# Kernel tuning notes

Measured on AMD Instinct MI355X. Metric: run time of the kernel, lower is better.

## Reference

```python
import jax, jax.numpy as jnp
import numpy as np

D_MODEL = 1024
N_SA = 8          # self-attention heads
N_RA = 8          # relational-attention heads
TOTAL = N_SA + N_RA
HEAD_DIM = D_MODEL // TOTAL   # 64
KEY_DIM = HEAD_DIM            # default key_dim = d_model // total_n_heads
N_REL = 8                     # n_relations (= n_heads_ra default)
REL_PROJ = KEY_DIM            # rel_proj_dim default
B, S = 4, 1024


def _rope(x, cos, sin):
    # x: [b, s, h, d]; cos/sin: [s, d//2]; interleaved-pair rotation as in apply_rotary_emb
    xr = x.reshape(x.shape[:-1] + (-1, 2))
    x_r, x_i = xr[..., 0], xr[..., 1]
    c = cos[None, :, None, :]
    s = sin[None, :, None, :]
    o_r = x_r * c - x_i * s
    o_i = x_r * s + x_i * c
    return jnp.stack([o_r, o_i], axis=-1).reshape(x.shape)


def setup_inputs() -> dict:
    key = jax.random.key(0)
    ks = jax.random.split(key, 16)
    def p(k, shape, scale=0.02):
        return jax.random.normal(k, shape, dtype=jnp.float32) * scale
    x = jax.random.normal(ks[0], (B, S, D_MODEL), dtype=jnp.float32)
    symbols = jax.random.normal(ks[1], (B, S, D_MODEL), dtype=jnp.float32)
    # standard RoPE frequency tables, shape [S, KEY_DIM//2]
    inv_freq = 1.0 / (10000.0 ** (np.arange(0, KEY_DIM, 2, dtype=np.float32) / KEY_DIM))
    ang = np.outer(np.arange(S, dtype=np.float32), inv_freq)
    freqs_cos = jnp.asarray(np.cos(ang), dtype=jnp.float32)
    freqs_sin = jnp.asarray(np.sin(ang), dtype=jnp.float32)
    return dict(
        x=x, symbols=symbols, freqs_cos=freqs_cos, freqs_sin=freqs_sin,
        # self-attention stream params
        wq_sa=p(ks[2], (D_MODEL, N_SA * KEY_DIM)),
        wk_sa=p(ks[3], (D_MODEL, N_SA * KEY_DIM)),
        wv_sa=p(ks[4], (D_MODEL, N_SA * HEAD_DIM)),
        wo_sa=p(ks[5], (N_SA * HEAD_DIM, N_SA * HEAD_DIM)),
        # relational-attention stream params
        wq_attn=p(ks[6], (D_MODEL, N_RA * KEY_DIM)),
        wk_attn=p(ks[7], (D_MODEL, N_RA * KEY_DIM)),
        wq_rel=p(ks[8], (D_MODEL, N_REL * REL_PROJ)),
        wk_rel=p(ks[9], (D_MODEL, N_REL * REL_PROJ)),
        wr=p(ks[10], (N_RA, HEAD_DIM, N_REL)),      # per-head relation->head_dim map
        wv_sym=p(ks[11], (D_MODEL, N_RA * HEAD_DIM)),  # symbol projection
        wo_ra=p(ks[12], (N_RA * HEAD_DIM, N_RA * HEAD_DIM)),
    )


def reference(x, symbols, freqs_cos, freqs_sin, wq_sa, wk_sa, wv_sa, wo_sa,
              wq_attn, wk_attn, wq_rel, wk_rel, wr, wv_sym, wo_ra):
    b, s, _ = x.shape
    attn_scale = 1.0 / jnp.sqrt(jnp.asarray(HEAD_DIM, dtype=x.dtype))
    rel_scale = 1.0 / jnp.sqrt(jnp.asarray(REL_PROJ, dtype=x.dtype))
    causal = jnp.tril(jnp.ones((s, s), dtype=bool))
    neg = jnp.where(causal, jnp.asarray(0.0, x.dtype), jnp.asarray(-jnp.inf, x.dtype))

    # ---- standard self-attention stream ----
    q = _rope((x @ wq_sa).reshape(b, s, N_SA, KEY_DIM), freqs_cos, freqs_sin)
    k = _rope((x @ wk_sa).reshape(b, s, N_SA, KEY_DIM), freqs_cos, freqs_sin)
    v = (x @ wv_sa).reshape(b, s, N_SA, HEAD_DIM)
    scores = jnp.einsum('bihd,bjhd->bhij', q, k) * attn_scale + neg
    attn = jax.nn.softmax(scores, axis=-1)
    sa_out = jnp.einsum('bhij,bjhd->bihd', attn, v).reshape(b, s, -1) @ wo_sa

    # ---- relational attention stream ----
    qa = _rope((x @ wq_attn).reshape(b, s, N_RA, KEY_DIM), freqs_cos, freqs_sin)
    ka = _rope((x @ wk_attn).reshape(b, s, N_RA, KEY_DIM), freqs_cos, freqs_sin)
    ra_scores = jnp.einsum('bihd,bjhd->bhij', qa, ka) * attn_scale + neg
    ra_attn = jax.nn.softmax(ra_scores, axis=-1)
    # relations r(i,j) in R^{n_rel}: inner products of relation projections, tanh-activated
    qr = (x @ wq_rel).reshape(b, s, N_REL, REL_PROJ)
    kr = (x @ wk_rel).reshape(b, s, N_REL, REL_PROJ)
    rel = jnp.tanh(jnp.einsum('bird,bjrd->bijr', qr, kr) * rel_scale)  # [b,s,s,n_rel]
    sv = (symbols @ wv_sym).reshape(b, s, N_RA, HEAD_DIM)
    sym_msg = jnp.einsum('bhij,bjhd->bihd', ra_attn, sv)
    rel_msg = jnp.einsum('bhij,bijr->bihr', ra_attn, rel)
    rel_proj = jnp.einsum('bihr,hdr->bihd', rel_msg, wr)
    ra_out = (sym_msg + rel_proj).reshape(b, s, -1) @ wo_ra

    # dual attention: concat the two streams along feature dim -> [b, s, d_model]
    return jnp.concatenate([sa_out, ra_out], axis=-1)
```

## Files before the change

### kernel.cpp

```cpp
#include <hip/hip_runtime.h>

typedef unsigned short u16;
typedef unsigned int u32;
typedef __attribute__((ext_vector_type(4))) short s16x4;
typedef __attribute__((ext_vector_type(8))) short s16x8;
typedef __attribute__((ext_vector_type(4))) float f32x4;

#define C_QSA 0
#define C_KSA 512
#define C_VSA 1024
#define C_QA  1536
#define C_KA  2048
#define C_QR  2560
#define C_KR  3072
#define C_SV  3584
#define LDP   4096

__device__ __forceinline__ u16 f2bf(float f) {
    union { float f; unsigned u; } v; v.f = f;
    return (u16)((v.u + 0x7FFFu + ((v.u >> 16) & 1u)) >> 16);
}
__device__ __forceinline__ float bf2f(u16 h) {
    union { unsigned u; float f; } v; v.u = ((unsigned)h) << 16; return v.f;
}
__device__ __forceinline__ float fexp(float y) {
    return __builtin_exp2f(y * 1.4426950408889634f);
}
__device__ __forceinline__ float ftanh(float x) {
    float e = __builtin_exp2f(x * 2.885390081777927f);
    return 1.f - 2.f / (e + 1.f);
}
__device__ __forceinline__ f32x4 mfma16(s16x8 a, s16x8 b, f32x4 c) {
    return __builtin_amdgcn_mfma_f32_16x16x32_bf16(a, b, c, 0, 0, 0);
}
__device__ __forceinline__ void gload16(const u16* g, u16* l) {
    __builtin_amdgcn_global_load_lds(
        (const __attribute__((address_space(1))) void*)g,
        (__attribute__((address_space(3))) void*)l, 16, 0, 0);
}


__global__ void cvt_f32_bf16(const float* __restrict__ in, u16* __restrict__ out, int n) {
    int i = (blockIdx.x * 256 + threadIdx.x) * 8;
    if (i >= n) return;
    float4 a = *(const float4*)(in + i);
    float4 b = *(const float4*)(in + i + 4);
    s16x8 o;
    o[0] = (short)f2bf(a.x); o[1] = (short)f2bf(a.y);
    o[2] = (short)f2bf(a.z); o[3] = (short)f2bf(a.w);
    o[4] = (short)f2bf(b.x); o[5] = (short)f2bf(b.y);
    o[6] = (short)f2bf(b.z); o[7] = (short)f2bf(b.w);
    *(s16x8*)(out + i) = o;
}

struct WP { const float* p[10]; };

__global__ void transpose_w(WP wp, u16* __restrict__ WcatT,
                            u16* __restrict__ woSaT, u16* __restrict__ woRaT) {
    const int z = blockIdx.z;
    const float* W;
    u16* Wt;
    int K;
    if (z < 8) { W = wp.p[z]; Wt = WcatT + (size_t)z * 524288; K = 1024; }
    else       { W = wp.p[z]; Wt = (z == 8) ? woSaT : woRaT;   K = 512;  }
    const int N = 512;
    const int kt = blockIdx.x * 32, nt = blockIdx.y * 32;
    if (kt >= K) return;
    __shared__ float t[32][33];
    const int c = threadIdx.x & 31, r0 = threadIdx.x >> 5;
#pragma unroll
    for (int it = 0; it < 4; ++it) {
        int r = it * 8 + r0;
        t[r][c] = W[(size_t)(kt + r) * N + nt + c];
    }
    __syncthreads();
#pragma unroll
    for (int it = 0; it < 4; ++it) {
        int r = it * 8 + r0;
        Wt[(size_t)(nt + r) * K + kt + c] = f2bf(t[c][r]);
    }
}

__global__ void transpose_v2(const u16* __restrict__ P, u16* __restrict__ Vt, int colOff) {
    const int st = blockIdx.x * 32, ht = blockIdx.y * 32, b = blockIdx.z;
    __shared__ u16 t[32][34];
    const int c = threadIdx.x & 31, r0 = threadIdx.x >> 5;
#pragma unroll
    for (int it = 0; it < 4; ++it) {
        int r = it * 8 + r0;
        t[r][c] = P[(size_t)(b * 1024 + st + r) * LDP + colOff + ht + c];
    }
    __syncthreads();
    const int cp = ((c & 15) >> 2) * 8 + (c >> 4) * 4 + (c & 3);
#pragma unroll
    for (int it = 0; it < 4; ++it) {
        int r = it * 8 + r0;
        Vt[(size_t)b * 524288 + (size_t)(ht + r) * 1024 + st + cp] = t[c][r];
    }
}


__global__ void rope_kernel(u16* __restrict__ P, const float* __restrict__ fcos,
                            const float* __restrict__ fsin) {
    int idx = blockIdx.x * 256 + threadIdx.x;
    int row = idx >> 10;
    int rem = idx & 1023;
    int region = rem >> 8;
    int pr = rem & 255;
    int head = pr >> 5, p = pr & 31;
    int off = (region + (region >> 1)) * 512;
    int col = off + head * 64 + 2 * p;
    int s = row & 1023;
    float c = fcos[s * 32 + p], sn = fsin[s * 32 + p];
    u32* ptr = (u32*)(P + (size_t)row * LDP + col);
    u32 v = *ptr;
    float xr = bf2f((u16)(v & 0xffff)), xi = bf2f((u16)(v >> 16));
    u16 o0 = f2bf(xr * c - xi * sn);
    u16 o1 = f2bf(xr * sn + xi * c);
    *ptr = (u32)o0 | ((u32)o1 << 16);
}


template<bool OUT_BF16>
__global__ __launch_bounds__(256) void gemm_bf16(
    const u16* __restrict__ A, const u16* __restrict__ A2, int lda, int nswitch,
    const u16* __restrict__ Bt, int ldb,
    void* __restrict__ Cp, int ldc, int ccolOff, int K)
{
    __shared__ u16 As[128][32];
    __shared__ u16 Bs[128][32];
    const int tid = threadIdx.x;
    const int m0 = blockIdx.x * 128, n0 = blockIdx.y * 128;
    const u16* Ause = (A2 != nullptr && n0 >= nswitch) ? A2 : A;
    const int w = tid >> 6, lane = tid & 63;
    const int w32 = w * 32;
    const int wm = (w >> 1) * 64, wn = (w & 1) * 64;
    const int lr = lane & 15, lg = lane >> 4;
    const int lrow = lane >> 2;
    const int lseg = (lane & 3) * 8;
    f32x4 acc[4][4] = {};

    for (int k0 = 0; k0 < K; k0 += 32) {
        const u16* ga = &Ause[(size_t)(m0 + w32 + lrow) * lda + k0 + lseg];
        const u16* gb = &Bt [(size_t)(n0 + w32 + lrow) * ldb + k0 + lseg];
        gload16(ga,            &As[w32][0]);
        gload16(ga + 16 * lda, &As[w32 + 16][0]);
        gload16(gb,            &Bs[w32][0]);
        gload16(gb + 16 * ldb, &Bs[w32 + 16][0]);
        __syncthreads();
        s16x8 af[4], bfr[4];
#pragma unroll
        for (int t = 0; t < 4; ++t) {
            af[t]  = *(const s16x8*)&As[wm + t * 16 + lr][lg * 8];
            bfr[t] = *(const s16x8*)&Bs[wn + t * 16 + lr][lg * 8];
        }
#pragma unroll
        for (int i = 0; i < 4; ++i)
#pragma unroll
            for (int j = 0; j < 4; ++j)
                acc[i][j] = mfma16(af[i], bfr[j], acc[i][j]);
        __syncthreads();
    }
#pragma unroll
    for (int i = 0; i < 4; ++i)
#pragma unroll
        for (int j = 0; j < 4; ++j)
#pragma unroll
            for (int r = 0; r < 4; ++r) {
                int row = m0 + wm + i * 16 + lg * 4 + r;
                int col = n0 + wn + j * 16 + lr;
                float val = acc[i][j][r];
                if (OUT_BF16)
                    ((u16*)Cp)[(size_t)row * ldc + ccolOff + col] = f2bf(val);
                else
                    ((float*)Cp)[(size_t)row * ldc + ccolOff + col] = val;
            }
}


__global__ __launch_bounds__(64) void attn_sa(u16* __restrict__ P, const u16* __restrict__ Vt) {
    const int bid = blockIdx.x;
    const int h = bid & 7;
    const int b = (bid >> 3) & 3;
    const int pr = bid >> 5;
    const int xt1 = pr, xt2 = 63 - pr;
    const int lane = threadIdx.x, lr = lane & 15, lg = lane >> 4;
    const size_t rowBase = (size_t)b * 1024;
    const int i0_1 = xt1 * 16, i0_2 = xt2 * 16;
    const int ir1 = i0_1 + lr, ir2 = i0_2 + lr;

    const u16* Kbase = P + rowBase * LDP + (C_KSA + h * 64);
    const u16* Vb = Vt + ((size_t)(b * 8 + h)) * 65536;

    s16x8 q1[2], q2[2];
    {
        const u16* q = P + (rowBase + ir1) * LDP + (C_QSA + h * 64) + lg * 8;
        q1[0] = *(const s16x8*)q; q1[1] = *(const s16x8*)(q + 32);
        q = P + (rowBase + ir2) * LDP + (C_QSA + h * 64) + lg * 8;
        q2[0] = *(const s16x8*)q; q2[1] = *(const s16x8*)(q + 32);
    }
    f32x4 o1[4] = {}, o2[4] = {};
    float l1 = 0.f, l2 = 0.f;
    const int njt  = (xt2 >> 1) + 1;
    const int njt1 = (xt1 >> 1) + 1;

    for (int jt = 0; jt < njt; ++jt) {
        const int j0 = jt * 32;
        const bool act1 = (jt < njt1);
        s16x8 kf[2][2], vfr[4];
#pragma unroll
        for (int sub = 0; sub < 2; ++sub) {
            const u16* kp = Kbase + (size_t)(j0 + sub * 16 + lr) * LDP + lg * 8;
            kf[sub][0] = *(const s16x8*)kp;
            kf[sub][1] = *(const s16x8*)(kp + 32);
        }
#pragma unroll
        for (int ds = 0; ds < 4; ++ds)
            vfr[ds] = *(const s16x8*)(Vb + (size_t)(ds * 16 + lr) * 1024 + j0 + 8 * lg);

        f32x4 sc2[2] = {{0.f,0.f,0.f,0.f},{0.f,0.f,0.f,0.f}};
        f32x4 sc1[2] = {{0.f,0.f,0.f,0.f},{0.f,0.f,0.f,0.f}};
#pragma unroll
        for (int sub = 0; sub < 2; ++sub) {
            sc2[sub] = mfma16(kf[sub][0], q2[0], sc2[sub]);
            sc2[sub] = mfma16(kf[sub][1], q2[1], sc2[sub]);
        }
        if (act1) {
#pragma unroll
            for (int sub = 0; sub < 2; ++sub) {
                sc1[sub] = mfma16(kf[sub][0], q1[0], sc1[sub]);
                sc1[sub] = mfma16(kf[sub][1], q1[1], sc1[sub]);
            }
        }
        s16x8 pa;
#pragma unroll
        for (int sub = 0; sub < 2; ++sub)
#pragma unroll
            for (int r = 0; r < 4; ++r) {
                int j = j0 + sub * 16 + 4 * lg + r;
                float p = (j <= ir2) ? fexp(sc2[sub][r] * 0.125f) : 0.f;
                l2 += p;
                pa[sub * 4 + r] = (short)f2bf(p);
            }
#pragma unroll
        for (int ds = 0; ds < 4; ++ds) o2[ds] = mfma16(pa, vfr[ds], o2[ds]);
        if (act1) {
#pragma unroll
            for (int sub = 0; sub < 2; ++sub)
#pragma unroll
                for (int r = 0; r < 4; ++r) {
                    int j = j0 + sub * 16 + 4 * lg + r;
                    float p = (j <= ir1) ? fexp(sc1[sub][r] * 0.125f) : 0.f;
                    l1 += p;
                    pa[sub * 4 + r] = (short)f2bf(p);
                }
#pragma unroll
            for (int ds = 0; ds < 4; ++ds) o1[ds] = mfma16(pa, vfr[ds], o1[ds]);
        }
    }
    l1 += __shfl_xor(l1, 16); l1 += __shfl_xor(l1, 32);
    l2 += __shfl_xor(l2, 16); l2 += __shfl_xor(l2, 32);
    float li1[4], li2[4];
#pragma unroll
    for (int r = 0; r < 4; ++r) {
        li1[r] = 1.f / __shfl(l1, 4 * lg + r);
        li2[r] = 1.f / __shfl(l2, 4 * lg + r);
    }
#pragma unroll
    for (int ds = 0; ds < 4; ++ds)
#pragma unroll
        for (int r = 0; r < 4; ++r) {
            P[(rowBase + i0_1 + 4 * lg + r) * LDP + (C_QSA + h * 64) + ds * 16 + lr] =
                f2bf(o1[ds][r] * li1[r]);
            P[(rowBase + i0_2 + 4 * lg + r) * LDP + (C_QSA + h * 64) + ds * 16 + lr] =
                f2bf(o2[ds][r] * li2[r]);
        }
}


__global__ __launch_bounds__(512) void attn_ra(u16* __restrict__ P, const u16* __restrict__ SVt,
                                               float* __restrict__ opart,
                                               float* __restrict__ mlr) {
    const int bid = blockIdx.x;
    const int slot = bid & 7;
    const int b = slot & 3, s = slot >> 2;
    const int xt = 63 - (bid >> 3);
    const int w = threadIdx.x >> 6, lane = threadIdx.x & 63;
    const int lr = lane & 15, lg = lane >> 4;
    const int h = w;
    const size_t rowBase = (size_t)b * 1024;
    const int i0 = xt * 16;
    const int ir = i0 + lr;

    __shared__ float relT[2][2][32][16][8];

    const u16* Kbase  = P + rowBase * LDP + (C_KA + h * 64);
    const u16* KRbase = P + rowBase * LDP + (C_KR + h * 64);
    const u16* Vb = SVt + ((size_t)(b * 8 + h)) * 65536;

    s16x8 qf[2], qrf[2];
    {
        const u16* q = P + (rowBase + ir) * LDP + (C_QA + h * 64) + lg * 8;
        qf[0] = *(const s16x8*)q; qf[1] = *(const s16x8*)(q + 32);
        const u16* qr = P + (rowBase + ir) * LDP + (C_QR + h * 64) + lg * 8;
        qrf[0] = *(const s16x8*)qr; qrf[1] = *(const s16x8*)(qr + 32);
    }
    f32x4 o[4] = {};
    float rmr[8] = {};
    float l = 0.f;
    const int njt = (xt >> 1) + 1;
    const int cnt = (njt - s + 1) >> 1;
    const int npair = (cnt + 1) >> 1;
    const int slotw = (w + lr) & 7;

    for (int u = 0; u < npair; ++u) {
        const int j0a = (s + 4 * u) * 32;
        const bool actB = (2 * u + 1) < cnt;
        const int j0b = actB ? j0a + 64 : j0a;
        s16x8 kfA[2][2], krA[2][2], kfB[2][2], krB[2][2], vfA[4], vfB[4];
#pragma unroll
        for (int sub = 0; sub < 2; ++sub) {
            const u16* kp = Kbase + (size_t)(j0a + sub * 16 + lr) * LDP + lg * 8;
            kfA[sub][0] = *(const s16x8*)kp;  kfA[sub][1] = *(const s16x8*)(kp + 32);
            const u16* krp = KRbase + (size_t)(j0a + sub * 16 + lr) * LDP + lg * 8;
            krA[sub][0] = *(const s16x8*)krp; krA[sub][1] = *(const s16x8*)(krp + 32);
            kp = Kbase + (size_t)(j0b + sub * 16 + lr) * LDP + lg * 8;
            kfB[sub][0] = *(const s16x8*)kp;  kfB[sub][1] = *(const s16x8*)(kp + 32);
            krp = KRbase + (size_t)(j0b + sub * 16 + lr) * LDP + lg * 8;
            krB[sub][0] = *(const s16x8*)krp; krB[sub][1] = *(const s16x8*)(krp + 32);
        }
#pragma unroll
        for (int ds = 0; ds < 4; ++ds) {
            vfA[ds] = *(const s16x8*)(Vb + (size_t)(ds * 16 + lr) * 1024 + j0a + 8 * lg);
            vfB[ds] = *(const s16x8*)(Vb + (size_t)(ds * 16 + lr) * 1024 + j0b + 8 * lg);
        }
        f32x4 scA[2] = {{0.f,0.f,0.f,0.f},{0.f,0.f,0.f,0.f}};
        f32x4 scB[2] = {{0.f,0.f,0.f,0.f},{0.f,0.f,0.f,0.f}};
        f32x4 rtA[2] = {{0.f,0.f,0.f,0.f},{0.f,0.f,0.f,0.f}};
        f32x4 rtB[2] = {{0.f,0.f,0.f,0.f},{0.f,0.f,0.f,0.f}};
#pragma unroll
        for (int sub = 0; sub < 2; ++sub) {
            scA[sub] = mfma16(kfA[sub][0], qf[0], scA[sub]);
            scA[sub] = mfma16(kfA[sub][1], qf[1], scA[sub]);
            rtA[sub] = mfma16(krA[sub][0], qrf[0], rtA[sub]);
            rtA[sub] = mfma16(krA[sub][1], qrf[1], rtA[sub]);
            scB[sub] = mfma16(kfB[sub][0], qf[0], scB[sub]);
            scB[sub] = mfma16(kfB[sub][1], qf[1], scB[sub]);
            rtB[sub] = mfma16(krB[sub][0], qrf[0], rtB[sub]);
            rtB[sub] = mfma16(krB[sub][1], qrf[1], rtB[sub]);
        }
        float pA[2][4], pB[2][4];
#pragma unroll
        for (int sub = 0; sub < 2; ++sub)
#pragma unroll
            for (int r = 0; r < 4; ++r) {
                int jA = j0a + sub * 16 + 4 * lg + r;
                int jB = j0b + sub * 16 + 4 * lg + r;
                pA[sub][r] = (jA <= ir) ? fexp(scA[sub][r] * 0.125f) : 0.f;
                pB[sub][r] = (actB && jB <= ir) ? fexp(scB[sub][r] * 0.125f) : 0.f;
                l += pA[sub][r] + pB[sub][r];
            }
#pragma unroll
        for (int sub = 0; sub < 2; ++sub)
#pragma unroll
            for (int r = 0; r < 4; ++r) {
                int jp = sub * 16 + 4 * lg + r;
                relT[u & 1][0][jp][lr][slotw] = ftanh(rtA[sub][r] * 0.125f);
                relT[u & 1][1][jp][lr][slotw] = ftanh(rtB[sub][r] * 0.125f);
            }
        __syncthreads();
#pragma unroll
        for (int sub = 0; sub < 2; ++sub)
#pragma unroll
            for (int r = 0; r < 4; ++r) {
                int jp = sub * 16 + 4 * lg + r;
                f32x4 a  = *(const f32x4*)&relT[u & 1][0][jp][lr][0];
                f32x4 bb = *(const f32x4*)&relT[u & 1][0][jp][lr][4];
                float pv = pA[sub][r];
#pragma unroll
                for (int k = 0; k < 4; ++k) {
                    rmr[k]     += pv * a[k];
                    rmr[4 + k] += pv * bb[k];
                }
                a  = *(const f32x4*)&relT[u & 1][1][jp][lr][0];
                bb = *(const f32x4*)&relT[u & 1][1][jp][lr][4];
                pv = pB[sub][r];
#pragma unroll
                for (int k = 0; k < 4; ++k) {
                    rmr[k]     += pv * a[k];
                    rmr[4 + k] += pv * bb[k];
                }
            }
        s16x8 paA, paB;
#pragma unroll
        for (int r = 0; r < 4; ++r) {
            paA[r]     = (short)f2bf(pA[0][r]);
            paA[4 + r] = (short)f2bf(pA[1][r]);
            paB[r]     = (short)f2bf(pB[0][r]);
            paB[4 + r] = (short)f2bf(pB[1][r]);
        }
#pragma unroll
        for (int ds = 0; ds < 4; ++ds) {
            o[ds] = mfma16(paA, vfA[ds], o[ds]);
            o[ds] = mfma16(paB, vfB[ds], o[ds]);
        }
    }

    l += __shfl_xor(l, 16); l += __shfl_xor(l, 32);
#pragma unroll
    for (int k = 0; k < 8; ++k) {
        float v = rmr[k];
        v += __shfl_xor(v, 16);
        v += __shfl_xor(v, 32);
        rmr[k] = v;
    }
    float g[8], t0[8];
    const int t = lr & 7;
#pragma unroll
    for (int k = 0; k < 8; ++k) g[k] = rmr[k];
#pragma unroll
    for (int k = 0; k < 8; ++k) t0[k] = (t & 1) ? g[(k + 1) & 7] : g[k];
#pragma unroll
    for (int k = 0; k < 8; ++k) g[k]  = (t & 2) ? t0[(k + 2) & 7] : t0[k];
#pragma unroll
    for (int k = 0; k < 8; ++k) t0[k] = (t & 4) ? g[(k + 4) & 7] : g[k];

    const int headRow = (b * 8 + h) * 1024;
#pragma unroll
    for (int ds = 0; ds < 4; ++ds)
#pragma unroll
        for (int r = 0; r < 4; ++r) {
            int row = headRow + i0 + 4 * lg + r;
            opart[((size_t)row * 2 + s) * 64 + ds * 16 + lr] = o[ds][r];
        }
    if (lg == 0) {
        float* pm = &mlr[((size_t)(headRow + i0 + lr) * 2 + s) * 10];
        pm[0] = l;
#pragma unroll
        for (int c = 0; c < 8; ++c) pm[1 + c] = t0[c];
    }
}


__global__ __launch_bounds__(256) void merge_ra(const float* __restrict__ opart,
                                                const float* __restrict__ mlr,
                                                const float* __restrict__ wr,
                                                u16* __restrict__ P) {
    const int gid = blockIdx.x * 4 + (threadIdx.x >> 6);
    const int d = threadIdx.x & 63;
    const int i = gid & 1023;
    const int h = (gid >> 10) & 7;
    const int b = gid >> 13;
    const float* ml0 = &mlr[(size_t)gid * 20];
    const float* ml1 = ml0 + 10;
    float ilt = 1.f / (ml0[0] + ml1[0]);
    float acc = (opart[(size_t)gid * 128 + d] +
                 opart[(size_t)gid * 128 + 64 + d]) * ilt;
#pragma unroll
    for (int c = 0; c < 8; ++c) {
        float rm = (ml0[1 + c] + ml1[1 + c]) * ilt;
        acc += rm * wr[h * 512 + d * 8 + c];
    }
    P[((size_t)(b * 1024 + i)) * LDP + C_QA + h * 64 + d] = f2bf(acc);
}


extern "C" void kernel_launch(void* const* d_in, const int* in_sizes, int n_in,
                              void* d_out, int out_size, void* d_ws, size_t ws_size,
                              hipStream_t stream)
{
    const float* x     = (const float*)d_in[0];
    const float* sym   = (const float*)d_in[1];
    const float* fcos  = (const float*)d_in[2];
    const float* fsin  = (const float*)d_in[3];
    const float* w_qsa = (const float*)d_in[4];
    const float* w_ksa = (const float*)d_in[5];
    const float* w_vsa = (const float*)d_in[6];
    const float* w_osa = (const float*)d_in[7];
    const float* w_qa  = (const float*)d_in[8];
    const float* w_ka  = (const float*)d_in[9];
    const float* w_qr  = (const float*)d_in[10];
    const float* w_kr  = (const float*)d_in[11];
    const float* wr    = (const float*)d_in[12];
    const float* w_sv  = (const float*)d_in[13];
    const float* w_ora = (const float*)d_in[14];

    char* ws = (char*)d_ws;
    u16* xb    = (u16*)(ws);
    u16* symb  = (u16*)(ws + (8u  << 20));
    u16* WcatT = (u16*)(ws + (16u << 20));
    u16* woSaT = (u16*)(ws + (24u << 20));
    u16* woRaT = (u16*)(ws + (24u << 20) + (512u << 10));
    u16* Pcat  = (u16*)(ws + (25u << 20));
    u16* vT    = (u16*)(ws + (57u << 20));
    u16* svT   = (u16*)(ws + (61u << 20));
    float* opart = (float*)(ws);
    float* mlrp  = (float*)(ws + (17u << 20));

    cvt_f32_bf16<<<2048, 256, 0, stream>>>(x,   xb,   4194304);
    cvt_f32_bf16<<<2048, 256, 0, stream>>>(sym, symb, 4194304);

    WP wp{{w_qsa, w_ksa, w_vsa, w_qa, w_ka, w_qr, w_kr, w_sv, w_osa, w_ora}};
    transpose_w<<<dim3(32, 16, 10), 256, 0, stream>>>(wp, WcatT, woSaT, woRaT);

    gemm_bf16<true><<<dim3(32, 32), 256, 0, stream>>>(
        xb, symb, 1024, C_SV, WcatT, 1024, Pcat, LDP, 0, 1024);

    rope_kernel<<<16384, 256, 0, stream>>>(Pcat, fcos, fsin);

    transpose_v2<<<dim3(32, 16, 4), 256, 0, stream>>>(Pcat, vT,  C_VSA);
    transpose_v2<<<dim3(32, 16, 4), 256, 0, stream>>>(Pcat, svT, C_SV);

    attn_sa<<<1024, 64, 0, stream>>>(Pcat, vT);
    attn_ra<<<512, 512, 0, stream>>>(Pcat, svT, opart, mlrp);
    merge_ra<<<8192, 256, 0, stream>>>(opart, mlrp, wr, Pcat);

    gemm_bf16<false><<<dim3(32, 8), 256, 0, stream>>>(
        Pcat + C_QSA, Pcat + C_QA, LDP, 512, woSaT, 512, d_out, 1024, 0, 512);
}
```

Measured before the change: 214.7 us.

## Split attention key loops across more waves and splits with bf16 partials

attn_sa now runs 4 waves per block, each taking every fourth key tile, and the per-wave partial outputs and row sums are reduced through shared memory. attn_ra now splits each query tile's keys four ways instead of two, and each block handles a pair of mirrored query tiles to balance causal work. Its partial outputs are stored as bf16 to cut memory traffic, and merge_ra sums four partials. The goal is more parallelism and better load balance, at the cost of extra reduction traffic, a block-wide barrier, and lower precision in the partial sums.

Measured after the change: 230.7 us. 7.5% more time.

```diff
diff --git a/kernel.cpp b/kernel.cpp
--- a/kernel.cpp
+++ b/kernel.cpp
@@ -178,16 +178,20 @@
 }
 
 
-__global__ __launch_bounds__(64) void attn_sa(u16* __restrict__ P, const u16* __restrict__ Vt) {
+__global__ __launch_bounds__(256) void attn_sa(u16* __restrict__ P, const u16* __restrict__ Vt) {
     const int bid = blockIdx.x;
     const int h = bid & 7;
     const int b = (bid >> 3) & 3;
     const int pr = bid >> 5;
+    const int w = threadIdx.x >> 6, lane = threadIdx.x & 63;
+    const int lr = lane & 15, lg = lane >> 4;
+    const size_t rowBase = (size_t)b * 1024;
     const int xt1 = pr, xt2 = 63 - pr;
-    const int lane = threadIdx.x, lr = lane & 15, lg = lane >> 4;
-    const size_t rowBase = (size_t)b * 1024;
     const int i0_1 = xt1 * 16, i0_2 = xt2 * 16;
     const int ir1 = i0_1 + lr, ir2 = i0_2 + lr;
+
+    __shared__ float oL[4][2][16][64];
+    __shared__ float lL[4][2][64];
 
     const u16* Kbase = P + rowBase * LDP + (C_KSA + h * 64);
     const u16* Vb = Vt + ((size_t)(b * 8 + h)) * 65536;
@@ -204,7 +208,7 @@
     const int njt  = (xt2 >> 1) + 1;
     const int njt1 = (xt1 >> 1) + 1;
 
-    for (int jt = 0; jt < njt; ++jt) {
+    for (int jt = w; jt < njt; jt += 4) {
         const int j0 = jt * 32;
         const bool act1 = (jt < njt1);
         s16x8 kf[2][2], vfr[4];
@@ -258,191 +262,214 @@
             for (int ds = 0; ds < 4; ++ds) o1[ds] = mfma16(pa, vfr[ds], o1[ds]);
         }
     }
-    l1 += __shfl_xor(l1, 16); l1 += __shfl_xor(l1, 32);
-    l2 += __shfl_xor(l2, 16); l2 += __shfl_xor(l2, 32);
-    float li1[4], li2[4];
-#pragma unroll
-    for (int r = 0; r < 4; ++r) {
-        li1[r] = 1.f / __shfl(l1, 4 * lg + r);
-        li2[r] = 1.f / __shfl(l2, 4 * lg + r);
-    }
 #pragma unroll
     for (int ds = 0; ds < 4; ++ds)
 #pragma unroll
         for (int r = 0; r < 4; ++r) {
-            P[(rowBase + i0_1 + 4 * lg + r) * LDP + (C_QSA + h * 64) + ds * 16 + lr] =
-                f2bf(o1[ds][r] * li1[r]);
-            P[(rowBase + i0_2 + 4 * lg + r) * LDP + (C_QSA + h * 64) + ds * 16 + lr] =
-                f2bf(o2[ds][r] * li2[r]);
-        }
+            oL[w][0][ds * 4 + r][lane] = o1[ds][r];
+            oL[w][1][ds * 4 + r][lane] = o2[ds][r];
+        }
+    lL[w][0][lane] = l1;
+    lL[w][1][lane] = l2;
+    __syncthreads();
+    if (w < 2) {
+        const int i0 = w ? i0_2 : i0_1;
+        f32x4 o[4];
+        float l = 0.f;
+#pragma unroll
+        for (int v = 0; v < 4; ++v) l += lL[v][w][lane];
+#pragma unroll
+        for (int ds = 0; ds < 4; ++ds)
+#pragma unroll
+            for (int r = 0; r < 4; ++r) {
+                float acc = 0.f;
+#pragma unroll
+                for (int v = 0; v < 4; ++v) acc += oL[v][w][ds * 4 + r][lane];
+                o[ds][r] = acc;
+            }
+        l += __shfl_xor(l, 16); l += __shfl_xor(l, 32);
+        float li[4];
+#pragma unroll
+        for (int r = 0; r < 4; ++r) li[r] = 1.f / __shfl(l, 4 * lg + r);
+#pragma unroll
+        for (int ds = 0; ds < 4; ++ds)
+#pragma unroll
+            for (int r = 0; r < 4; ++r)
+                P[(rowBase + i0 + 4 * lg + r) * LDP + (C_QSA + h * 64) + ds * 16 + lr] =
+                    f2bf(o[ds][r] * li[r]);
+    }
 }
 
 
 __global__ __launch_bounds__(512) void attn_ra(u16* __restrict__ P, const u16* __restrict__ SVt,
-                                               float* __restrict__ opart,
+                                               u16* __restrict__ opart,
                                                float* __restrict__ mlr) {
     const int bid = blockIdx.x;
-    const int slot = bid & 7;
-    const int b = slot & 3, s = slot >> 2;
-    const int xt = 63 - (bid >> 3);
+    const int b = bid & 3;
+    const int s = (bid >> 2) & 3;
+    const int pr = bid >> 4;
     const int w = threadIdx.x >> 6, lane = threadIdx.x & 63;
     const int lr = lane & 15, lg = lane >> 4;
     const int h = w;
     const size_t rowBase = (size_t)b * 1024;
-    const int i0 = xt * 16;
-    const int ir = i0 + lr;
+    const int slotw = (w + lr) & 7;
 
     __shared__ float relT[2][2][32][16][8];
 
     const u16* Kbase  = P + rowBase * LDP + (C_KA + h * 64);
     const u16* KRbase = P + rowBase * LDP + (C_KR + h * 64);
     const u16* Vb = SVt + ((size_t)(b * 8 + h)) * 65536;
-
-    s16x8 qf[2], qrf[2];
-    {
-        const u16* q = P + (rowBase + ir) * LDP + (C_QA + h * 64) + lg * 8;
-        qf[0] = *(const s16x8*)q; qf[1] = *(const s16x8*)(q + 32);
-        const u16* qr = P + (rowBase + ir) * LDP + (C_QR + h * 64) + lg * 8;
-        qrf[0] = *(const s16x8*)qr; qrf[1] = *(const s16x8*)(qr + 32);
-    }
-    f32x4 o[4] = {};
-    float rmr[8] = {};
-    float l = 0.f;
-    const int njt = (xt >> 1) + 1;
-    const int cnt = (njt - s + 1) >> 1;
-    const int npair = (cnt + 1) >> 1;
-    const int slotw = (w + lr) & 7;
-
-    for (int u = 0; u < npair; ++u) {
-        const int j0a = (s + 4 * u) * 32;
-        const bool actB = (2 * u + 1) < cnt;
-        const int j0b = actB ? j0a + 64 : j0a;
-        s16x8 kfA[2][2], krA[2][2], kfB[2][2], krB[2][2], vfA[4], vfB[4];
-#pragma unroll
-        for (int sub = 0; sub < 2; ++sub) {
-            const u16* kp = Kbase + (size_t)(j0a + sub * 16 + lr) * LDP + lg * 8;
-            kfA[sub][0] = *(const s16x8*)kp;  kfA[sub][1] = *(const s16x8*)(kp + 32);
-            const u16* krp = KRbase + (size_t)(j0a + sub * 16 + lr) * LDP + lg * 8;
-            krA[sub][0] = *(const s16x8*)krp; krA[sub][1] = *(const s16x8*)(krp + 32);
-            kp = Kbase + (size_t)(j0b + sub * 16 + lr) * LDP + lg * 8;
-            kfB[sub][0] = *(const s16x8*)kp;  kfB[sub][1] = *(const s16x8*)(kp + 32);
-            krp = KRbase + (size_t)(j0b + sub * 16 + lr) * LDP + lg * 8;
-            krB[sub][0] = *(const s16x8*)krp; krB[sub][1] = *(const s16x8*)(krp + 32);
-        }
-#pragma unroll
-        for (int ds = 0; ds < 4; ++ds) {
-            vfA[ds] = *(const s16x8*)(Vb + (size_t)(ds * 16 + lr) * 1024 + j0a + 8 * lg);
-            vfB[ds] = *(const s16x8*)(Vb + (size_t)(ds * 16 + lr) * 1024 + j0b + 8 * lg);
-        }
-        f32x4 scA[2] = {{0.f,0.f,0.f,0.f},{0.f,0.f,0.f,0.f}};
-        f32x4 scB[2] = {{0.f,0.f,0.f,0.f},{0.f,0.f,0.f,0.f}};
-        f32x4 rtA[2] = {{0.f,0.f,0.f,0.f},{0.f,0.f,0.f,0.f}};
-        f32x4 rtB[2] = {{0.f,0.f,0.f,0.f},{0.f,0.f,0.f,0.f}};
-#pragma unroll
-        for (int sub = 0; sub < 2; ++sub) {
-            scA[sub] = mfma16(kfA[sub][0], qf[0], scA[sub]);
-            scA[sub] = mfma16(kfA[sub][1], qf[1], scA[sub]);
-            rtA[sub] = mfma16(krA[sub][0], qrf[0], rtA[sub]);
-            rtA[sub] = mfma16(krA[sub][1], qrf[1], rtA[sub]);
-            scB[sub] = mfma16(kfB[sub][0], qf[0], scB[sub]);
-            scB[sub] = mfma16(kfB[sub][1], qf[1], scB[sub]);
-            rtB[sub] = mfma16(krB[sub][0], qrf[0], rtB[sub]);
-            rtB[sub] = mfma16(krB[sub][1], qrf[1], rtB[sub]);
-        }
-        float pA[2][4], pB[2][4];
-#pragma unroll
-        for (int sub = 0; sub < 2; ++sub)
+    int db = 0;
+
+    for (int tsel = 0; tsel < 2; ++tsel) {
+        const int xt = tsel ? 63 - pr : pr;
+        const int i0 = xt * 16;
+        const int ir = i0 + lr;
+        s16x8 qf[2], qrf[2];
+        {
+            const u16* q = P + (rowBase + ir) * LDP + (C_QA + h * 64) + lg * 8;
+            qf[0] = *(const s16x8*)q; qf[1] = *(const s16x8*)(q + 32);
+            const u16* qr = P + (rowBase + ir) * LDP + (C_QR + h * 64) + lg * 8;
+            qrf[0] = *(const s16x8*)qr; qrf[1] = *(const s16x8*)(qr + 32);
+        }
+        f32x4 o[4] = {};
+        float rmr[8] = {};
+        float l = 0.f;
+        const int njt = (xt >> 1) + 1;
+        const int cnt = (njt > s) ? ((njt - s + 3) >> 2) : 0;
+        const int npair = (cnt + 1) >> 1;
+
+        for (int u = 0; u < npair; ++u, db ^= 1) {
+            const int j0a = (s + 8 * u) * 32;
+            const bool actB = (2 * u + 1) < cnt;
+            const int j0b = actB ? j0a + 128 : j0a;
+            s16x8 kfA[2][2], krA[2][2], kfB[2][2], krB[2][2], vfA[4], vfB[4];
+#pragma unroll
+            for (int sub = 0; sub < 2; ++sub) {
+                const u16* kp = Kbase + (size_t)(j0a + sub * 16 + lr) * LDP + lg * 8;
+                kfA[sub][0] = *(const s16x8*)kp;  kfA[sub][1] = *(const s16x8*)(kp + 32);
+                const u16* krp = KRbase + (size_t)(j0a + sub * 16 + lr) * LDP + lg * 8;
+                krA[sub][0] = *(const s16x8*)krp; krA[sub][1] = *(const s16x8*)(krp + 32);
+                kp = Kbase + (size_t)(j0b + sub * 16 + lr) * LDP + lg * 8;
+                kfB[sub][0] = *(const s16x8*)kp;  kfB[sub][1] = *(const s16x8*)(kp + 32);
+                krp = KRbase + (size_t)(j0b + sub * 16 + lr) * LDP + lg * 8;
+                krB[sub][0] = *(const s16x8*)krp; krB[sub][1] = *(const s16x8*)(krp + 32);
+            }
+#pragma unroll
+            for (int ds = 0; ds < 4; ++ds) {
+                vfA[ds] = *(const s16x8*)(Vb + (size_t)(ds * 16 + lr) * 1024 + j0a + 8 * lg);
+                vfB[ds] = *(const s16x8*)(Vb + (size_t)(ds * 16 + lr) * 1024 + j0b + 8 * lg);
+            }
+            f32x4 scA[2] = {{0.f,0.f,0.f,0.f},{0.f,0.f,0.f,0.f}};
+            f32x4 scB[2] = {{0.f,0.f,0.f,0.f},{0.f,0.f,0.f,0.f}};
+            f32x4 rtA[2] = {{0.f,0.f,0.f,0.f},{0.f,0.f,0.f,0.f}};
+            f32x4 rtB[2] = {{0.f,0.f,0.f,0.f},{0.f,0.f,0.f,0.f}};
+#pragma unroll
+            for (int sub = 0; sub < 2; ++sub) {
+                scA[sub] = mfma16(kfA[sub][0], qf[0], scA[sub]);
+                scA[sub] = mfma16(kfA[sub][1], qf[1], scA[sub]);
+                rtA[sub] = mfma16(krA[sub][0], qrf[0], rtA[sub]);
+                rtA[sub] = mfma16(krA[sub][1], qrf[1], rtA[sub]);
+                scB[sub] = mfma16(kfB[sub][0], qf[0], scB[sub]);
+                scB[sub] = mfma16(kfB[sub][1], qf[1], scB[sub]);
+                rtB[sub] = mfma16(krB[sub][0], qrf[0], rtB[sub]);
+                rtB[sub] = mfma16(krB[sub][1], qrf[1], rtB[sub]);
+            }
+            float pA[2][4], pB[2][4];
+#pragma unroll
+            for (int sub = 0; sub < 2; ++sub)
+#pragma unroll
+                for (int r = 0; r < 4; ++r) {
+                    int jA = j0a + sub * 16 + 4 * lg + r;
+                    int jB = j0b + sub * 16 + 4 * lg + r;
+                    pA[sub][r] = (jA <= ir) ? fexp(scA[sub][r] * 0.125f) : 0.f;
+                    pB[sub][r] = (actB && jB <= ir) ? fexp(scB[sub][r] * 0.125f) : 0.f;
+                    l += pA[sub][r] + pB[sub][r];
+                }
+#pragma unroll
+            for (int sub = 0; sub < 2; ++sub)
+#pragma unroll
+                for (int r = 0; r < 4; ++r) {
+                    int jp = sub * 16 + 4 * lg + r;
+                    relT[db][0][jp][lr][slotw] = ftanh(rtA[sub][r] * 0.125f);
+                    relT[db][1][jp][lr][slotw] = ftanh(rtB[sub][r] * 0.125f);
+                }
+            __syncthreads();
+#pragma unroll
+            for (int sub = 0; sub < 2; ++sub)
+#pragma unroll
+                for (int r = 0; r < 4; ++r) {
+                    int jp = sub * 16 + 4 * lg + r;
+                    f32x4 a  = *(const f32x4*)&relT[db][0][jp][lr][0];
+                    f32x4 bb = *(const f32x4*)&relT[db][0][jp][lr][4];
+                    float pv = pA[sub][r];
+#pragma unroll
+                    for (int k = 0; k < 4; ++k) {
+                        rmr[k]     += pv * a[k];
+                        rmr[4 + k] += pv * bb[k];
+                    }
+                    a  = *(const f32x4*)&relT[db][1][jp][lr][0];
+                    bb = *(const f32x4*)&relT[db][1][jp][lr][4];
+                    pv = pB[sub][r];
+#pragma unroll
+                    for (int k = 0; k < 4; ++k) {
+                        rmr[k]     += pv * a[k];
+                        rmr[4 + k] += pv * bb[k];
+                    }
+                }
+            s16x8 paA, paB;
 #pragma unroll
             for (int r = 0; r < 4; ++r) {
-                int jA = j0a + sub * 16 + 4 * lg + r;
-                int jB = j0b + sub * 16 + 4 * lg + r;
-                pA[sub][r] = (jA <= ir) ? fexp(scA[sub][r] * 0.125f) : 0.f;
-                pB[sub][r] = (actB && jB <= ir) ? fexp(scB[sub][r] * 0.125f) : 0.f;
-                l += pA[sub][r] + pB[sub][r];
-            }
-#pragma unroll
-        for (int sub = 0; sub < 2; ++sub)
+                paA[r]     = (short)f2bf(pA[0][r]);
+                paA[4 + r] = (short)f2bf(pA[1][r]);
+                paB[r]     = (short)f2bf(pB[0][r]);
+                paB[4 + r] = (short)f2bf(pB[1][r]);
+            }
+#pragma unroll
+            for (int ds = 0; ds < 4; ++ds) {
+                o[ds] = mfma16(paA, vfA[ds], o[ds]);
+                o[ds] = mfma16(paB, vfB[ds], o[ds]);
+            }
+        }
+
+        l += __shfl_xor(l, 16); l += __shfl_xor(l, 32);
+#pragma unroll
+        for (int k = 0; k < 8; ++k) {
+            float v = rmr[k];
+            v += __shfl_xor(v, 16);
+            v += __shfl_xor(v, 32);
+            rmr[k] = v;
+        }
+        float g[8], t0[8];
+        const int t = lr & 7;
+#pragma unroll
+        for (int k = 0; k < 8; ++k) g[k] = rmr[k];
+#pragma unroll
+        for (int k = 0; k < 8; ++k) t0[k] = (t & 1) ? g[(k + 1) & 7] : g[k];
+#pragma unroll
+        for (int k = 0; k < 8; ++k) g[k]  = (t & 2) ? t0[(k + 2) & 7] : t0[k];
+#pragma unroll
+        for (int k = 0; k < 8; ++k) t0[k] = (t & 4) ? g[(k + 4) & 7] : g[k];
+
+        const int headRow = (b * 8 + h) * 1024;
+#pragma unroll
+        for (int ds = 0; ds < 4; ++ds)
 #pragma unroll
             for (int r = 0; r < 4; ++r) {
-                int jp = sub * 16 + 4 * lg + r;
-                relT[u & 1][0][jp][lr][slotw] = ftanh(rtA[sub][r] * 0.125f);
-                relT[u & 1][1][jp][lr][slotw] = ftanh(rtB[sub][r] * 0.125f);
-            }
-        __syncthreads();
-#pragma unroll
-        for (int sub = 0; sub < 2; ++sub)
-#pragma unroll
-            for (int r = 0; r < 4; ++r) {
-                int jp = sub * 16 + 4 * lg + r;
-                f32x4 a  = *(const f32x4*)&relT[u & 1][0][jp][lr][0];
-                f32x4 bb = *(const f32x4*)&relT[u & 1][0][jp][lr][4];
-                float pv = pA[sub][r];
-#pragma unroll
-                for (int k = 0; k < 4; ++k) {
-                    rmr[k]     += pv * a[k];
-                    rmr[4 + k] += pv * bb[k];
-                }
-                a  = *(const f32x4*)&relT[u & 1][1][jp][lr][0];
-                bb = *(const f32x4*)&relT[u & 1][1][jp][lr][4];
-                pv = pB[sub][r];
-#pragma unroll
-                for (int k = 0; k < 4; ++k) {
-                    rmr[k]     += pv * a[k];
-                    rmr[4 + k] += pv * bb[k];
-                }
-            }
-        s16x8 paA, paB;
-#pragma unroll
-        for (int r = 0; r < 4; ++r) {
-            paA[r]     = (short)f2bf(pA[0][r]);
-            paA[4 + r] = (short)f2bf(pA[1][r]);
-            paB[r]     = (short)f2bf(pB[0][r]);
-            paB[4 + r] = (short)f2bf(pB[1][r]);
-        }
-#pragma unroll
-        for (int ds = 0; ds < 4; ++ds) {
-            o[ds] = mfma16(paA, vfA[ds], o[ds]);
-            o[ds] = mfma16(paB, vfB[ds], o[ds]);
-        }
-    }
-
-    l += __shfl_xor(l, 16); l += __shfl_xor(l, 32);
-#pragma unroll
-    for (int k = 0; k < 8; ++k) {
-        float v = rmr[k];
-        v += __shfl_xor(v, 16);
-        v += __shfl_xor(v, 32);
-        rmr[k] = v;
-    }
-    float g[8], t0[8];
-    const int t = lr & 7;
-#pragma unroll
-    for (int k = 0; k < 8; ++k) g[k] = rmr[k];
-#pragma unroll
-    for (int k = 0; k < 8; ++k) t0[k] = (t & 1) ? g[(k + 1) & 7] : g[k];
-#pragma unroll
-    for (int k = 0; k < 8; ++k) g[k]  = (t & 2) ? t0[(k + 2) & 7] : t0[k];
-#pragma unroll
-    for (int k = 0; k < 8; ++k) t0[k] = (t & 4) ? g[(k + 4) & 7] : g[k];
-
-    const int headRow = (b * 8 + h) * 1024;
-#pragma unroll
-    for (int ds = 0; ds < 4; ++ds)
-#pragma unroll
-        for (int r = 0; r < 4; ++r) {
-            int row = headRow + i0 + 4 * lg + r;
-            opart[((size_t)row * 2 + s) * 64 + ds * 16 + lr] = o[ds][r];
-        }
-    if (lg == 0) {
-        float* pm = &mlr[((size_t)(headRow + i0 + lr) * 2 + s) * 10];
-        pm[0] = l;
-#pragma unroll
-        for (int c = 0; c < 8; ++c) pm[1 + c] = t0[c];
-    }
-}
-
-
-__global__ __launch_bounds__(256) void merge_ra(const float* __restrict__ opart,
+                int row = headRow + i0 + 4 * lg + r;
+                opart[(size_t)row * 256 + s * 64 + ds * 16 + lr] = f2bf(o[ds][r]);
+            }
+        if (lg == 0) {
+            float* pm = &mlr[((size_t)(headRow + i0 + lr) * 4 + s) * 9];
+            pm[0] = l;
+#pragma unroll
+            for (int c = 0; c < 8; ++c) pm[1 + c] = t0[c];
+        }
+    }
+}
+
+
+__global__ __launch_bounds__(256) void merge_ra(const u16* __restrict__ opart,
                                                 const float* __restrict__ mlr,
                                                 const float* __restrict__ wr,
                                                 u16* __restrict__ P) {
@@ -451,16 +478,20 @@
     const int i = gid & 1023;
     const int h = (gid >> 10) & 7;
     const int b = gid >> 13;
-    const float* ml0 = &mlr[(size_t)gid * 20];
-    const float* ml1 = ml0 + 10;
-    float ilt = 1.f / (ml0[0] + ml1[0]);
-    float acc = (opart[(size_t)gid * 128 + d] +
-                 opart[(size_t)gid * 128 + 64 + d]) * ilt;
-#pragma unroll
-    for (int c = 0; c < 8; ++c) {
-        float rm = (ml0[1 + c] + ml1[1 + c]) * ilt;
-        acc += rm * wr[h * 512 + d * 8 + c];
-    }
+    float lt = 0.f, osum = 0.f, rm[8] = {};
+#pragma unroll
+    for (int s = 0; s < 4; ++s) {
+        const float* pm = &mlr[((size_t)gid * 4 + s) * 9];
+        lt += pm[0];
+#pragma unroll
+        for (int c = 0; c < 8; ++c) rm[c] += pm[1 + c];
+        osum += bf2f(opart[(size_t)gid * 256 + s * 64 + d]);
+    }
+    float ilt = 1.f / lt;
+    float acc = osum * ilt;
+#pragma unroll
+    for (int c = 0; c < 8; ++c)
+        acc += rm[c] * ilt * wr[h * 512 + d * 8 + c];
     P[((size_t)(b * 1024 + i)) * LDP + C_QA + h * 64 + d] = f2bf(acc);
 }
 
@@ -494,7 +525,7 @@
     u16* Pcat  = (u16*)(ws + (25u << 20));
     u16* vT    = (u16*)(ws + (57u << 20));
     u16* svT   = (u16*)(ws + (61u << 20));
-    float* opart = (float*)(ws);
+    u16*   opart = (u16*)(ws);
     float* mlrp  = (float*)(ws + (17u << 20));
 
     cvt_f32_bf16<<<2048, 256, 0, stream>>>(x,   xb,   4194304);
@@ -511,7 +542,7 @@
     transpose_v2<<<dim3(32, 16, 4), 256, 0, stream>>>(Pcat, vT,  C_VSA);
     transpose_v2<<<dim3(32, 16, 4), 256, 0, stream>>>(Pcat, svT, C_SV);
 
-    attn_sa<<<1024, 64, 0, stream>>>(Pcat, vT);
+    attn_sa<<<1024, 256, 0, stream>>>(Pcat, vT);
     attn_ra<<<512, 512, 0, stream>>>(Pcat, svT, opart, mlrp);
     merge_ra<<<8192, 256, 0, stream>>>(opart, mlrp, wr, Pcat);
 
```

## Split relational attention KV range four ways and store partials in bf16

Applied to the files above, without the earlier changes.

The relational attention kernel now divides each query tile's key range across four blocks instead of two, doubling the grid to 1024 blocks for more parallelism on the causal workload. The partial output accumulators are stored as bf16 instead of fp32 to cut the extra write/read traffic, and the merge kernel sums four partials. This adds more merge work and per-block fixed overhead, and loses precision in the partial sums.

Result: slower. 230.1 us (+7.2%).

```diff
diff --git a/kernel.cpp b/kernel.cpp
--- a/kernel.cpp
+++ b/kernel.cpp
@@ -279,18 +279,19 @@
 
 
 __global__ __launch_bounds__(512) void attn_ra(u16* __restrict__ P, const u16* __restrict__ SVt,
-                                               float* __restrict__ opart,
+                                               u16* __restrict__ opart,
                                                float* __restrict__ mlr) {
     const int bid = blockIdx.x;
-    const int slot = bid & 7;
-    const int b = slot & 3, s = slot >> 2;
-    const int xt = 63 - (bid >> 3);
+    const int b = bid & 3;
+    const int s = (bid >> 2) & 3;
+    const int xt = 63 - (bid >> 4);
     const int w = threadIdx.x >> 6, lane = threadIdx.x & 63;
     const int lr = lane & 15, lg = lane >> 4;
     const int h = w;
     const size_t rowBase = (size_t)b * 1024;
     const int i0 = xt * 16;
     const int ir = i0 + lr;
+    const int slotw = (w + lr) & 7;
 
     __shared__ float relT[2][2][32][16][8];
 
@@ -309,14 +310,13 @@
     float rmr[8] = {};
     float l = 0.f;
     const int njt = (xt >> 1) + 1;
-    const int cnt = (njt - s + 1) >> 1;
+    const int cnt = (njt > s) ? ((njt - s + 3) >> 2) : 0;
     const int npair = (cnt + 1) >> 1;
-    const int slotw = (w + lr) & 7;
 
     for (int u = 0; u < npair; ++u) {
-        const int j0a = (s + 4 * u) * 32;
+        const int j0a = (s + 8 * u) * 32;
         const bool actB = (2 * u + 1) < cnt;
-        const int j0b = actB ? j0a + 64 : j0a;
+        const int j0b = actB ? j0a + 128 : j0a;
         s16x8 kfA[2][2], krA[2][2], kfB[2][2], krB[2][2], vfA[4], vfB[4];
 #pragma unroll
         for (int sub = 0; sub < 2; ++sub) {
@@ -360,13 +360,14 @@
                 pB[sub][r] = (actB && jB <= ir) ? fexp(scB[sub][r] * 0.125f) : 0.f;
                 l += pA[sub][r] + pB[sub][r];
             }
+        const int db = u & 1;
 #pragma unroll
         for (int sub = 0; sub < 2; ++sub)
 #pragma unroll
             for (int r = 0; r < 4; ++r) {
                 int jp = sub * 16 + 4 * lg + r;
-                relT[u & 1][0][jp][lr][slotw] = ftanh(rtA[sub][r] * 0.125f);
-                relT[u & 1][1][jp][lr][slotw] = ftanh(rtB[sub][r] * 0.125f);
+                relT[db][0][jp][lr][slotw] = ftanh(rtA[sub][r] * 0.125f);
+                relT[db][1][jp][lr][slotw] = ftanh(rtB[sub][r] * 0.125f);
             }
         __syncthreads();
 #pragma unroll
@@ -374,16 +375,16 @@
 #pragma unroll
             for (int r = 0; r < 4; ++r) {
                 int jp = sub * 16 + 4 * lg + r;
-                f32x4 a  = *(const f32x4*)&relT[u & 1][0][jp][lr][0];
-                f32x4 bb = *(const f32x4*)&relT[u & 1][0][jp][lr][4];
+                f32x4 a  = *(const f32x4*)&relT[db][0][jp][lr][0];
+                f32x4 bb = *(const f32x4*)&relT[db][0][jp][lr][4];
                 float pv = pA[sub][r];
 #pragma unroll
                 for (int k = 0; k < 4; ++k) {
                     rmr[k]     += pv * a[k];
                     rmr[4 + k] += pv * bb[k];
                 }
-                a  = *(const f32x4*)&relT[u & 1][1][jp][lr][0];
-                bb = *(const f32x4*)&relT[u & 1][1][jp][lr][4];
+                a  = *(const f32x4*)&relT[db][1][jp][lr][0];
+                bb = *(const f32x4*)&relT[db][1][jp][lr][4];
                 pv = pB[sub][r];
 #pragma unroll
                 for (int k = 0; k < 4; ++k) {
@@ -431,10 +432,10 @@
 #pragma unroll
         for (int r = 0; r < 4; ++r) {
             int row = headRow + i0 + 4 * lg + r;
-            opart[((size_t)row * 2 + s) * 64 + ds * 16 + lr] = o[ds][r];
+            opart[(size_t)row * 256 + s * 64 + ds * 16 + lr] = f2bf(o[ds][r]);
         }
     if (lg == 0) {
-        float* pm = &mlr[((size_t)(headRow + i0 + lr) * 2 + s) * 10];
+        float* pm = &mlr[((size_t)(headRow + i0 + lr) * 4 + s) * 9];
         pm[0] = l;
 #pragma unroll
         for (int c = 0; c < 8; ++c) pm[1 + c] = t0[c];
@@ -442,7 +443,7 @@
 }
 
 
-__global__ __launch_bounds__(256) void merge_ra(const float* __restrict__ opart,
+__global__ __launch_bounds__(256) void merge_ra(const u16* __restrict__ opart,
                                                 const float* __restrict__ mlr,
                                                 const float* __restrict__ wr,
                                                 u16* __restrict__ P) {
@@ -451,16 +452,20 @@
     const int i = gid & 1023;
     const int h = (gid >> 10) & 7;
     const int b = gid >> 13;
-    const float* ml0 = &mlr[(size_t)gid * 20];
-    const float* ml1 = ml0 + 10;
-    float ilt = 1.f / (ml0[0] + ml1[0]);
-    float acc = (opart[(size_t)gid * 128 + d] +
-                 opart[(size_t)gid * 128 + 64 + d]) * ilt;
-#pragma unroll
-    for (int c = 0; c < 8; ++c) {
-        float rm = (ml0[1 + c] + ml1[1 + c]) * ilt;
-        acc += rm * wr[h * 512 + d * 8 + c];
-    }
+    float lt = 0.f, osum = 0.f, rm[8] = {};
+#pragma unroll
+    for (int s = 0; s < 4; ++s) {
+        const float* pm = &mlr[((size_t)gid * 4 + s) * 9];
+        lt += pm[0];
+#pragma unroll
+        for (int c = 0; c < 8; ++c) rm[c] += pm[1 + c];
+        osum += bf2f(opart[(size_t)gid * 256 + s * 64 + d]);
+    }
+    float ilt = 1.f / lt;
+    float acc = osum * ilt;
+#pragma unroll
+    for (int c = 0; c < 8; ++c)
+        acc += rm[c] * ilt * wr[h * 512 + d * 8 + c];
     P[((size_t)(b * 1024 + i)) * LDP + C_QA + h * 64 + d] = f2bf(acc);
 }
 
@@ -494,7 +499,7 @@
     u16* Pcat  = (u16*)(ws + (25u << 20));
     u16* vT    = (u16*)(ws + (57u << 20));
     u16* svT   = (u16*)(ws + (61u << 20));
-    float* opart = (float*)(ws);
+    u16*   opart = (u16*)(ws);
     float* mlrp  = (float*)(ws + (17u << 20));
 
     cvt_f32_bf16<<<2048, 256, 0, stream>>>(x,   xb,   4194304);
@@ -512,7 +517,7 @@
     transpose_v2<<<dim3(32, 16, 4), 256, 0, stream>>>(Pcat, svT, C_SV);
 
     attn_sa<<<1024, 64, 0, stream>>>(Pcat, vT);
-    attn_ra<<<512, 512, 0, stream>>>(Pcat, svT, opart, mlrp);
+    attn_ra<<<1024, 512, 0, stream>>>(Pcat, svT, opart, mlrp);
     merge_ra<<<8192, 256, 0, stream>>>(opart, mlrp, wr, Pcat);
 
     gemm_bf16<false><<<dim3(32, 8), 256, 0, stream>>>(
```

## Fuse RoPE into projection GEMM epilogue and merge input conversions

Applied to the files above, without the earlier changes.

Removes the standalone RoPE kernel by applying the rotation in the projection GEMM epilogue, using a lane shuffle to fetch the paired column. This avoids a read-modify-write pass over the Q/K regions. The two f32-to-bf16 conversion launches are merged into one. GEMM workgroup indices are also remapped across groups of 8, which is intended to improve cache locality across XCDs.

New measurement: 227.6 us. +6.0%, slower.

```diff
diff --git a/kernel.cpp b/kernel.cpp
--- a/kernel.cpp
+++ b/kernel.cpp
@@ -40,17 +40,21 @@
 }
 
 
-__global__ void cvt_f32_bf16(const float* __restrict__ in, u16* __restrict__ out, int n) {
+__global__ void cvt2_f32_bf16(const float* __restrict__ a, const float* __restrict__ b,
+                              u16* __restrict__ oa, u16* __restrict__ ob) {
     int i = (blockIdx.x * 256 + threadIdx.x) * 8;
-    if (i >= n) return;
-    float4 a = *(const float4*)(in + i);
-    float4 b = *(const float4*)(in + i + 4);
+    const int half = (i >= 4194304) ? 1 : 0;
+    const float* in = half ? b : a;
+    u16* out = half ? ob : oa;
+    int off = i - half * 4194304;
+    float4 x = *(const float4*)(in + off);
+    float4 y = *(const float4*)(in + off + 4);
     s16x8 o;
-    o[0] = (short)f2bf(a.x); o[1] = (short)f2bf(a.y);
-    o[2] = (short)f2bf(a.z); o[3] = (short)f2bf(a.w);
-    o[4] = (short)f2bf(b.x); o[5] = (short)f2bf(b.y);
-    o[6] = (short)f2bf(b.z); o[7] = (short)f2bf(b.w);
-    *(s16x8*)(out + i) = o;
+    o[0] = (short)f2bf(x.x); o[1] = (short)f2bf(x.y);
+    o[2] = (short)f2bf(x.z); o[3] = (short)f2bf(x.w);
+    o[4] = (short)f2bf(y.x); o[5] = (short)f2bf(y.y);
+    o[6] = (short)f2bf(y.z); o[7] = (short)f2bf(y.w);
+    *(s16x8*)(out + off) = o;
 }
 
 struct WP { const float* p[10]; };
@@ -100,37 +104,22 @@
 }
 
 
-__global__ void rope_kernel(u16* __restrict__ P, const float* __restrict__ fcos,
-                            const float* __restrict__ fsin) {
-    int idx = blockIdx.x * 256 + threadIdx.x;
-    int row = idx >> 10;
-    int rem = idx & 1023;
-    int region = rem >> 8;
-    int pr = rem & 255;
-    int head = pr >> 5, p = pr & 31;
-    int off = (region + (region >> 1)) * 512;
-    int col = off + head * 64 + 2 * p;
-    int s = row & 1023;
-    float c = fcos[s * 32 + p], sn = fsin[s * 32 + p];
-    u32* ptr = (u32*)(P + (size_t)row * LDP + col);
-    u32 v = *ptr;
-    float xr = bf2f((u16)(v & 0xffff)), xi = bf2f((u16)(v >> 16));
-    u16 o0 = f2bf(xr * c - xi * sn);
-    u16 o1 = f2bf(xr * sn + xi * c);
-    *ptr = (u32)o0 | ((u32)o1 << 16);
-}
-
-
-template<bool OUT_BF16>
+template<bool OUT_BF16, bool DO_ROPE>
 __global__ __launch_bounds__(256) void gemm_bf16(
     const u16* __restrict__ A, const u16* __restrict__ A2, int lda, int nswitch,
     const u16* __restrict__ Bt, int ldb,
-    void* __restrict__ Cp, int ldc, int ccolOff, int K)
+    void* __restrict__ Cp, int ldc, int ccolOff, int K,
+    const float* __restrict__ fcos, const float* __restrict__ fsin)
 {
     __shared__ u16 As[128][32];
     __shared__ u16 Bs[128][32];
     const int tid = threadIdx.x;
-    const int m0 = blockIdx.x * 128, n0 = blockIdx.y * 128;
+    const int nwg = gridDim.x * gridDim.y;
+    const int lin = blockIdx.y * gridDim.x + blockIdx.x;
+    const int newlin = (lin & 7) * (nwg >> 3) + (lin >> 3);
+    const int bx = newlin % gridDim.x;
+    const int by = newlin / gridDim.x;
+    const int m0 = bx * 128, n0 = by * 128;
     const u16* Ause = (A2 != nullptr && n0 >= nswitch) ? A2 : A;
     const int w = tid >> 6, lane = tid & 63;
     const int w32 = w * 32;
@@ -164,17 +153,27 @@
 #pragma unroll
     for (int i = 0; i < 4; ++i)
 #pragma unroll
-        for (int j = 0; j < 4; ++j)
+        for (int j = 0; j < 4; ++j) {
+            const int colBase = n0 + wn + j * 16;
+            const bool rope = DO_ROPE && ((0x1B >> (colBase >> 9)) & 1);
 #pragma unroll
             for (int r = 0; r < 4; ++r) {
                 int row = m0 + wm + i * 16 + lg * 4 + r;
-                int col = n0 + wn + j * 16 + lr;
+                int col = colBase + lr;
                 float val = acc[i][j][r];
+                if (rope) {
+                    int p = (col & 63) >> 1;
+                    int sidx = (row & 1023) * 32 + p;
+                    float c = fcos[sidx], sn = fsin[sidx];
+                    float pv = __shfl_xor(val, 1);
+                    val = (col & 1) ? (pv * sn + val * c) : (val * c - pv * sn);
+                }
                 if (OUT_BF16)
                     ((u16*)Cp)[(size_t)row * ldc + ccolOff + col] = f2bf(val);
                 else
                     ((float*)Cp)[(size_t)row * ldc + ccolOff + col] = val;
             }
+        }
 }
 
 
@@ -497,16 +496,13 @@
     float* opart = (float*)(ws);
     float* mlrp  = (float*)(ws + (17u << 20));
 
-    cvt_f32_bf16<<<2048, 256, 0, stream>>>(x,   xb,   4194304);
-    cvt_f32_bf16<<<2048, 256, 0, stream>>>(sym, symb, 4194304);
+    cvt2_f32_bf16<<<4096, 256, 0, stream>>>(x, sym, xb, symb);
 
     WP wp{{w_qsa, w_ksa, w_vsa, w_qa, w_ka, w_qr, w_kr, w_sv, w_osa, w_ora}};
     transpose_w<<<dim3(32, 16, 10), 256, 0, stream>>>(wp, WcatT, woSaT, woRaT);
 
-    gemm_bf16<true><<<dim3(32, 32), 256, 0, stream>>>(
-        xb, symb, 1024, C_SV, WcatT, 1024, Pcat, LDP, 0, 1024);
-
-    rope_kernel<<<16384, 256, 0, stream>>>(Pcat, fcos, fsin);
+    gemm_bf16<true, true><<<dim3(32, 32), 256, 0, stream>>>(
+        xb, symb, 1024, C_SV, WcatT, 1024, Pcat, LDP, 0, 1024, fcos, fsin);
 
     transpose_v2<<<dim3(32, 16, 4), 256, 0, stream>>>(Pcat, vT,  C_VSA);
     transpose_v2<<<dim3(32, 16, 4), 256, 0, stream>>>(Pcat, svT, C_SV);
@@ -515,6 +511,7 @@
     attn_ra<<<512, 512, 0, stream>>>(Pcat, svT, opart, mlrp);
     merge_ra<<<8192, 256, 0, stream>>>(opart, mlrp, wr, Pcat);
 
-    gemm_bf16<false><<<dim3(32, 8), 256, 0, stream>>>(
-        Pcat + C_QSA, Pcat + C_QA, LDP, 512, woSaT, 512, d_out, 1024, 0, 512);
-}
+    gemm_bf16<false, false><<<dim3(32, 8), 256, 0, stream>>>(
+        Pcat + C_QSA, Pcat + C_QA, LDP, 512, woSaT, 512, d_out, 1024, 0, 512,
+        nullptr, nullptr);
+}
```
